# Kernel optimization log

Measured on AMD Instinct MI355X. Metric: run time of the kernel, lower is better.

## Reference

```python
import jax, jax.numpy as jnp
import numpy as np

H = 128          # hidden_size
D2 = 2 * H       # mod / q_enc channels
D8 = 8 * H       # att channels
B, S, G, Q = 16, 4096, 24, 48
WIN = 12         # +/- window half-width from source


def _masked_softmax(s, m, axis):
    s = jnp.where(m.astype(bool), s, jnp.float32(-1e30))
    return jax.nn.softmax(s, axis=axis)


def _bidaf(c, q, c_mask, q_mask, c_w, q_w, cq_w, bias):
    # c: [B,Lc,D2], q: [B,Lq,D2]; eval mode -> dropout is identity
    s0 = c @ c_w                                  # [B,Lc,1]
    s1 = (q @ q_w).transpose(0, 2, 1)             # [B,1,Lq]
    s2 = jnp.einsum('bcd,bqd->bcq', c * cq_w, q)  # [B,Lc,Lq]
    s = s0 + s1 + s2 + bias
    sm1 = _masked_softmax(s, q_mask[:, None, :], 2)
    sm2 = _masked_softmax(s, c_mask[:, :, None], 1)
    a = jnp.einsum('bcq,bqd->bcd', sm1, q)
    ss = jnp.einsum('bcq,bkq->bck', sm1, sm2)     # s1 @ s2^T
    b = jnp.einsum('bck,bkd->bcd', ss, c)
    return jnp.concatenate([c, a, c * a, c * b], axis=-1)  # [B,Lc,4*D2]


def setup_inputs() -> dict:
    key = jax.random.key(0)
    ks = jax.random.split(key, 12)
    inp = {
        'att': jax.random.normal(ks[0], (B, S, D8), jnp.float32),
        'mod': jax.random.normal(ks[1], (B, S, D2), jnp.float32),
        'q_enc': jax.random.normal(ks[2], (B, Q, D2), jnp.float32),
        'gap_indices': jnp.sort(jax.random.randint(ks[3], (B, G), 0, S), axis=1).astype(jnp.int32),
        'mask': jnp.ones((B, S), jnp.int32),
        'q_mask': jnp.ones((B, Q), jnp.int32),
        'c_w': jax.random.normal(ks[4], (D2, 1), jnp.float32) * 0.05,
        'q_w': jax.random.normal(ks[5], (D2, 1), jnp.float32) * 0.05,
        'cq_w': jax.random.normal(ks[6], (D2,), jnp.float32) * 0.05,
        'att_bias': jnp.zeros((1,), jnp.float32),
        'W_att': jax.random.normal(ks[7], (3 * D8, 1), jnp.float32) * 0.02,
        'b_att': jnp.zeros((1,), jnp.float32),
        'W_mod': jax.random.normal(ks[8], (3 * D2, 1), jnp.float32) * 0.02,
        'b_mod': jnp.zeros((1,), jnp.float32),
        'W_att2': jax.random.normal(ks[9], (D8, 1), jnp.float32) * 0.02,
        'b_att2': jnp.zeros((1,), jnp.float32),
        'W_att_s': jax.random.normal(ks[10], (3 * D8, 1), jnp.float32) * 0.02,
        'b_att_s': jnp.zeros((1,), jnp.float32),
        'W_mod_s': jax.random.normal(ks[11], (3 * D2, 1), jnp.float32) * 0.02,
        'b_mod_s': jnp.zeros((1,), jnp.float32),
        'W_att_s2': jax.random.normal(jax.random.fold_in(key, 99), (D8, 1), jnp.float32) * 0.02,
        'b_att_s2': jnp.zeros((1,), jnp.float32),
    }
    return inp


def reference(att, mod, q_enc, gap_indices, mask, q_mask,
              c_w, q_w, cq_w, att_bias,
              W_att, b_att, W_mod, b_mod, W_att2, b_att2,
              W_att_s, b_att_s, W_mod_s, b_mod_s, W_att_s2, b_att_s2):
    batch, seq_len, _ = mod.shape
    idxb = jnp.arange(batch)[:, None]
    att_gaps = att[idxb, gap_indices]   # [B,G,D8]
    mod_gaps = mod[idxb, gap_indices]   # [B,G,D2]

    att_2 = _bidaf(mod_gaps, q_enc, jnp.ones_like(gap_indices), q_mask,
                   c_w, q_w, cq_w, att_bias)  # [B,G,8h]

    # gap 0: full-sequence pooling (max is unmasked in the source; avg uses mask sum)
    denom0 = jnp.sum(mask.astype(jnp.float32), axis=1)[:, None]
    p0_mod = jnp.concatenate([jnp.max(mod, axis=1), jnp.sum(mod, axis=1) / denom0], axis=-1)[:, None]
    p0_att = jnp.concatenate([jnp.max(att, axis=1), jnp.sum(att, axis=1) / denom0], axis=-1)[:, None]

    pos = jnp.arange(seq_len)[None, :]
    mask_b = mask.astype(bool)

    def step(carry, gid):  # gid: [B]
        wm = (pos >= gid[:, None] - WIN) & (pos <= gid[:, None] + WIN) & mask_b
        wmf = wm.astype(jnp.float32)                 # [B,S]
        den = jnp.sum(wmf, axis=1)[:, None]          # [B,1]
        mw = mod * wmf[:, :, None]
        aw = att * wmf[:, :, None]
        pm = jnp.concatenate([jnp.max(mw, axis=1), jnp.sum(mw, axis=1) / den], axis=-1)
        pa = jnp.concatenate([jnp.max(aw, axis=1), jnp.sum(aw, axis=1) / den], axis=-1)
        return carry, (pm, pa)

    _, (pm, pa) = jax.lax.scan(step, None, gap_indices[:, 1:].T)  # [G-1,B,*]
    pools_mod = jnp.concatenate([p0_mod, pm.transpose(1, 0, 2)], axis=1)  # [B,G,4h]
    pools_att = jnp.concatenate([p0_att, pa.transpose(1, 0, 2)], axis=1)  # [B,G,16h]

    mod_g = jnp.concatenate([mod_gaps, pools_mod], axis=-1)  # [B,G,6h]
    att_g = jnp.concatenate([att_gaps, pools_att], axis=-1)  # [B,G,24h]

    lin = lambda x, W, b: x @ W + b
    logit0 = lin(att_g[:, :1], W_att_s, b_att_s) + lin(mod_g[:, :1], W_mod_s, b_mod_s) + lin(att_2[:, :1], W_att_s2, b_att_s2)
    logits = lin(att_g[:, 1:], W_att, b_att) + lin(mod_g[:, 1:], W_mod, b_mod) + lin(att_2[:, 1:], W_att2, b_att2)
    return jnp.concatenate([logit0, logits], axis=1).squeeze(-1)  # [B,G]
```

## Files before the change

### kernel.cpp

```cpp
#include <hip/hip_runtime.h>
#include <math.h>

#define BATCH 16
#define S_LEN 4096
#define D2c   256
#define D8c   1024
#define GNUM  24
#define QNUM  48
#define WINc  12
#define NCA   64
#define NCM   16
#define NSB   (BATCH * GNUM)
#define NWB   (BATCH * (GNUM - 1))

__device__ inline float4 f4max(float4 a, float4 b) {
    return make_float4(fmaxf(a.x,b.x), fmaxf(a.y,b.y), fmaxf(a.z,b.z), fmaxf(a.w,b.w));
}
__device__ inline float4 f4add(float4 a, float4 b) {
    return make_float4(a.x+b.x, a.y+b.y, a.z+b.z, a.w+b.w);
}
__device__ inline float4 f4scale(float4 a, float s) {
    return make_float4(a.x*s, a.y*s, a.z*s, a.w*s);
}
__device__ inline float4 f4mul(float4 a, float4 b) {
    return make_float4(a.x*b.x, a.y*b.y, a.z*b.z, a.w*b.w);
}
__device__ inline float dot4(float4 a, float4 b) {
    return a.x*b.x + a.y*b.y + a.z*b.z + a.w*b.w;
}
__device__ inline unsigned fmap(float x) {
    unsigned u = __float_as_uint(x);
    return (u >> 31) ? ~u : (u | 0x80000000u);
}
__device__ inline float funmap(unsigned u) {
    return (u >> 31) ? __uint_as_float(u & 0x7FFFFFFFu) : __uint_as_float(~u);
}

struct SSh {
    float c[D2c];
    float pa[4][QNUM];
    float pb[4][QNUM];
    float pm[8][32];
    float p0[2][64];
    int   gids[GNUM];
};
struct WSh {
    float wmf[32];
    float red[256];
    float rden;
};
union ShU { SSh s; WSh w; };

__global__ __launch_bounds__(256) void k1_kernel(
    const float* __restrict__ att, const float* __restrict__ mod,
    const float* __restrict__ q_enc,
    const int* __restrict__ gap_idx, const int* __restrict__ mask,
    const float* __restrict__ c_w, const float* __restrict__ cq_w,
    const float* __restrict__ W_att2, const float* __restrict__ W_att_s2,
    const float* __restrict__ W_att, const float* __restrict__ W_mod,
    const float* __restrict__ W_att_s, const float* __restrict__ W_mod_s,
    unsigned* __restrict__ attMaxU, unsigned* __restrict__ modMaxU,
    float* __restrict__ sumdots,
    float* __restrict__ s2v_ws, float* __restrict__ vv_ws,
    float* __restrict__ m_ws, float* __restrict__ s0uc_ws,
    float* __restrict__ winpart)
{
    __shared__ ShU sh;
    const int tid = threadIdx.x;
    const int bid = blockIdx.x;

    if (bid < NSB) {
        const int b = bid / GNUM, g = bid % GNUM;
        const float4* mod4 = reinterpret_cast<const float4*>(mod);
        const float4* q4   = reinterpret_cast<const float4*>(q_enc);
        const float4* Wsel = reinterpret_cast<const float4*>((g == 0) ? W_att_s2 : W_att2);

        if (tid < GNUM) sh.s.gids[tid] = gap_idx[b * GNUM + tid];
        __syncthreads();
        const int gid = sh.s.gids[g];
        if (tid < 64)
            reinterpret_cast<float4*>(sh.s.c)[tid] = mod4[((size_t)b * S_LEN + gid) * (D2c/4) + tid];
        __syncthreads();
        const float4* c4 = reinterpret_cast<const float4*>(sh.s.c);

        if (tid < 64) {
            sh.s.p0[0][tid] = dot4(c4[tid], reinterpret_cast<const float4*>(c_w)[tid]);
        } else if (tid < 128) {
            sh.s.p0[1][tid - 64] = dot4(c4[tid - 64], Wsel[tid - 64]);
        }

        {
            const int q = tid & 63, p = tid >> 6;
            if (q < QNUM) {
                const float4* qr = q4 + ((size_t)b * QNUM + q) * (D2c/4) + p * 16;
                const float4* cl = c4 + p * 16;
                const float4* cw = reinterpret_cast<const float4*>(cq_w) + p * 16;
                const float4* wa = Wsel + 2 * (D2c/4) + p * 16;
                float a_s2 = 0.f, a_v = 0.f;
                #pragma unroll
                for (int i = 0; i < 16; ++i) {
                    const float4 cq = f4mul(cl[i], qr[i]);
                    a_s2 += dot4(cq, cw[i]);
                    a_v  += dot4(cq, wa[i]);
                }
                sh.s.pa[p][q] = a_s2;
                sh.s.pb[p][q] = a_v;
            }
        }

        {
            const int k = tid & 31, p8 = tid >> 5;
            if (k < GNUM) {
                const float4* kr = mod4 + ((size_t)b * S_LEN + sh.s.gids[k]) * (D2c/4) + p8 * 8;
                const float4* cl = c4 + p8 * 8;
                const float4* wb = Wsel + 3 * (D2c/4) + p8 * 8;
                float am = 0.f;
                #pragma unroll
                for (int i = 0; i < 8; ++i) {
                    const float4 t = f4mul(cl[i], kr[i]);
                    am += dot4(t, wb[i]);
                }
                sh.s.pm[p8][k] = am;
            }
        }
        __syncthreads();

        if (tid < QNUM) {
            const float s2 = sh.s.pa[0][tid] + sh.s.pa[1][tid] + sh.s.pa[2][tid] + sh.s.pa[3][tid];
            const float v  = sh.s.pb[0][tid] + sh.s.pb[1][tid] + sh.s.pb[2][tid] + sh.s.pb[3][tid];
            s2v_ws[(size_t)bid * QNUM + tid] = s2;
            vv_ws [(size_t)bid * QNUM + tid] = v;
        } else if (tid >= 64 && tid < 64 + GNUM) {
            const int k = tid - 64;
            float m = 0.f;
            #pragma unroll
            for (int p8 = 0; p8 < 8; ++p8) m += sh.s.pm[p8][k];
            m_ws[(size_t)bid * GNUM + k] = m;
        } else if (tid == 62) {
            float a = 0.f;
            for (int i = 0; i < 64; ++i) a += sh.s.p0[0][i];
            s0uc_ws[(size_t)bid * 2 + 0] = a;
        } else if (tid == 63) {
            float a = 0.f;
            for (int i = 0; i < 64; ++i) a += sh.s.p0[1][i];
            s0uc_ws[(size_t)bid * 2 + 1] = a;
        }
    } else if (bid < NSB + NWB) {
        const int wb = bid - NSB;
        const int b = wb / (GNUM - 1), g = wb % (GNUM - 1) + 1;
        const int gid = gap_idx[b * GNUM + g];
        const int lo = (gid - WINc > 0) ? gid - WINc : 0;
        const int hi = (gid + WINc < S_LEN - 1) ? gid + WINc : S_LEN - 1;
        const int n = hi - lo + 1;
        const int gsel = gid - lo;

        if (tid < 32)
            sh.w.wmf[tid] = (tid < n && mask[b * S_LEN + lo + tid] != 0) ? 1.f : 0.f;
        __syncthreads();
        if (tid == 0) {
            float d = 0.f;
            for (int i = 0; i < 25; ++i) d += sh.w.wmf[i];
            sh.w.rden = 1.f / d;
        }
        __syncthreads();
        const float rden = sh.w.rden;

        const float4* Wa4 = reinterpret_cast<const float4*>(W_att);
        const float4* Wm4 = reinterpret_cast<const float4*>(W_mod);

        float acc = 0.f;
        {
            const float4* base = reinterpret_cast<const float4*>(att)
                                 + ((size_t)b * S_LEN + lo) * (D8c/4) + tid;
            float4 mx = make_float4(0.f, 0.f, 0.f, 0.f);
            float4 sm = make_float4(0.f, 0.f, 0.f, 0.f);
            float4 gv = make_float4(0.f, 0.f, 0.f, 0.f);
            #pragma unroll 5
            for (int i = 0; i < 25; ++i) {
                const int off = (i < n) ? i : 0;
                const float4 v = base[(size_t)off * (D8c/4)];
                const float w = sh.w.wmf[i];
                const float4 vm = f4scale(v, w);
                mx = f4max(mx, vm);
                sm = f4add(sm, vm);
                if (i == gsel) gv = v;
            }
            acc += dot4(gv, Wa4[tid]);
            acc += dot4(mx, Wa4[(D8c/4) + tid]) + dot4(sm, Wa4[2*(D8c/4) + tid]) * rden;
        }
        if (tid < D2c/4) {
            const float4* base = reinterpret_cast<const float4*>(mod)
                                 + ((size_t)b * S_LEN + lo) * (D2c/4) + tid;
            float4 mx = make_float4(0.f, 0.f, 0.f, 0.f);
            float4 sm = make_float4(0.f, 0.f, 0.f, 0.f);
            float4 gv = make_float4(0.f, 0.f, 0.f, 0.f);
            #pragma unroll 5
            for (int i = 0; i < 25; ++i) {
                const int off = (i < n) ? i : 0;
                const float4 v = base[(size_t)off * (D2c/4)];
                const float w = sh.w.wmf[i];
                const float4 vm = f4scale(v, w);
                mx = f4max(mx, vm);
                sm = f4add(sm, vm);
                if (i == gsel) gv = v;
            }
            acc += dot4(gv, Wm4[tid]);
            acc += dot4(mx, Wm4[(D2c/4) + tid]) + dot4(sm, Wm4[2*(D2c/4) + tid]) * rden;
        }

        sh.w.red[tid] = acc;
        __syncthreads();
        for (int off = 128; off > 0; off >>= 1) {
            if (tid < off) sh.w.red[tid] += sh.w.red[tid + off];
            __syncthreads();
        }
        if (tid == 0) winpart[b * GNUM + g] = sh.w.red[0];
    } else if (bid < NSB + NWB + BATCH * NCA) {
        const int ab = bid - NSB - NWB;
        const int b = ab >> 6, ch = ab & 63;
        const float4* base = reinterpret_cast<const float4*>(att)
                             + ((size_t)b * S_LEN + ch * 64) * (D8c/4) + tid;
        float4 mx = make_float4(-INFINITY, -INFINITY, -INFINITY, -INFINITY);
        float4 sm = make_float4(0.f, 0.f, 0.f, 0.f);
        #pragma unroll 8
        for (int r = 0; r < 64; ++r) {
            const float4 v = base[(size_t)r * (D8c/4)];
            mx = f4max(mx, v);
            sm = f4add(sm, v);
        }
        unsigned* amax = attMaxU + (size_t)b * D8c + tid * 4;
        atomicMax(&amax[0], fmap(mx.x));
        atomicMax(&amax[1], fmap(mx.y));
        atomicMax(&amax[2], fmap(mx.z));
        atomicMax(&amax[3], fmap(mx.w));
        const float4 wsum = reinterpret_cast<const float4*>(W_att_s)[2*(D8c/4) + tid];
        sh.w.red[tid] = dot4(sm, wsum);
        __syncthreads();
        for (int off = 128; off > 0; off >>= 1) {
            if (tid < off) sh.w.red[tid] += sh.w.red[tid + off];
            __syncthreads();
        }
        if (tid == 0) atomicAdd(&sumdots[b], sh.w.red[0]);
    } else {
        const int mb = bid - NSB - NWB - BATCH * NCA;
        const int b = mb >> 4, ch = mb & 15;
        const int rg = tid >> 6, c4i = tid & 63;
        const float4* base = reinterpret_cast<const float4*>(mod)
                             + ((size_t)b * S_LEN + ch * 256 + rg * 64) * (D2c/4) + c4i;
        float4 mx = make_float4(-INFINITY, -INFINITY, -INFINITY, -INFINITY);
        float4 sm = make_float4(0.f, 0.f, 0.f, 0.f);
        #pragma unroll 8
        for (int r = 0; r < 64; ++r) {
            const float4 v = base[(size_t)r * (D2c/4)];
            mx = f4max(mx, v);
            sm = f4add(sm, v);
        }
        unsigned* mmax = modMaxU + (size_t)b * D2c + c4i * 4;
        atomicMax(&mmax[0], fmap(mx.x));
        atomicMax(&mmax[1], fmap(mx.y));
        atomicMax(&mmax[2], fmap(mx.z));
        atomicMax(&mmax[3], fmap(mx.w));
        const float4 wsum = reinterpret_cast<const float4*>(W_mod_s)[2*(D2c/4) + c4i];
        sh.w.red[tid] = dot4(sm, wsum);
        __syncthreads();
        for (int off = 128; off > 0; off >>= 1) {
            if (tid < off) sh.w.red[tid] += sh.w.red[tid + off];
            __syncthreads();
        }
        if (tid == 0) atomicAdd(&sumdots[BATCH + b], sh.w.red[0]);
    }
}

__global__ __launch_bounds__(256) void k2_kernel(
    const float* __restrict__ att, const float* __restrict__ mod,
    const float* __restrict__ q_enc,
    const int* __restrict__ gap_idx, const int* __restrict__ mask,
    const int* __restrict__ q_mask,
    const float* __restrict__ q_w, const float* __restrict__ att_bias,
    const float* __restrict__ W_att2, const float* __restrict__ W_att_s2,
    const float* __restrict__ W_att_s, const float* __restrict__ W_mod_s,
    const float* __restrict__ b_att, const float* __restrict__ b_mod,
    const float* __restrict__ b_att2,
    const float* __restrict__ b_att_s, const float* __restrict__ b_mod_s,
    const float* __restrict__ b_att_s2,
    const unsigned* __restrict__ attMaxU, const unsigned* __restrict__ modMaxU,
    const float* __restrict__ sumdots,
    const float* __restrict__ s2v_ws, const float* __restrict__ vv_ws,
    const float* __restrict__ m_ws, const float* __restrict__ s0uc_ws,
    const float* __restrict__ winpart,
    float* __restrict__ out)
{
    const int b = blockIdx.x;
    const int tid = threadIdx.x;

    __shared__ float s_sh[GNUM][QNUM];
    __shared__ float sm1[GNUM][QNUM];
    __shared__ float sm2[GNUM][QNUM];
    __shared__ float ssm[GNUM][GNUM];
    __shared__ float pq[3][4][QNUM];
    __shared__ float s1[QNUM], u0[QNUM], u1[QNUM];
    __shared__ float s0g[GNUM], ucg[GNUM], att2v[GNUM];
    __shared__ float red[256];
    __shared__ float rdensh;

    {
        const int q = tid & 63, p = tid >> 6;
        if (q < QNUM) {
            const float4* qr = reinterpret_cast<const float4*>(q_enc)
                               + ((size_t)b * QNUM + q) * (D2c/4) + p * 16;
            const float4* w1 = reinterpret_cast<const float4*>(q_w) + p * 16;
            const float4* w2 = reinterpret_cast<const float4*>(W_att_s2) + (D2c/4) + p * 16;
            const float4* w3 = reinterpret_cast<const float4*>(W_att2)   + (D2c/4) + p * 16;
            float a1 = 0.f, a2 = 0.f, a3 = 0.f;
            #pragma unroll
            for (int i = 0; i < 16; ++i) {
                const float4 v = qr[i];
                a1 += dot4(v, w1[i]);
                a2 += dot4(v, w2[i]);
                a3 += dot4(v, w3[i]);
            }
            pq[0][p][q] = a1; pq[1][p][q] = a2; pq[2][p][q] = a3;
        }
    }
    if (tid < GNUM) {
        s0g[tid] = s0uc_ws[((size_t)b * GNUM + tid) * 2 + 0];
        ucg[tid] = s0uc_ws[((size_t)b * GNUM + tid) * 2 + 1];
    }
    __syncthreads();
    if (tid < QNUM) {
        s1[tid] = pq[0][0][tid] + pq[0][1][tid] + pq[0][2][tid] + pq[0][3][tid];
        u0[tid] = pq[1][0][tid] + pq[1][1][tid] + pq[1][2][tid] + pq[1][3][tid];
        u1[tid] = pq[2][0][tid] + pq[2][1][tid] + pq[2][2][tid] + pq[2][3][tid];
    }
    __syncthreads();

    const float bias = att_bias[0];
    for (int i = tid; i < GNUM * QNUM; i += 256) {
        const int g = i / QNUM, q = i % QNUM;
        s_sh[g][q] = s0g[g] + s1[q] + s2v_ws[((size_t)b * GNUM + g) * QNUM + q] + bias;
    }
    __syncthreads();

    if (tid < QNUM) {
        const int q = tid;
        float mxv = -1e30f;
        for (int g = 0; g < GNUM; ++g) mxv = fmaxf(mxv, s_sh[g][q]);
        float sum = 0.f;
        for (int g = 0; g < GNUM; ++g) {
            const float e = __expf(s_sh[g][q] - mxv);
            sm2[g][q] = e;
            sum += e;
        }
        const float inv = 1.f / sum;
        for (int g = 0; g < GNUM; ++g) sm2[g][q] *= inv;
    } else if (tid >= 64 && tid < 64 + GNUM) {
        const int g = tid - 64;
        float mxv = -1e30f;
        for (int q = 0; q < QNUM; ++q)
            if (q_mask[b * QNUM + q]) mxv = fmaxf(mxv, s_sh[g][q]);
        float sum = 0.f;
        for (int q = 0; q < QNUM; ++q) {
            const float e = q_mask[b * QNUM + q] ? __expf(s_sh[g][q] - mxv) : 0.f;
            sm1[g][q] = e;
            sum += e;
        }
        const float inv = 1.f / sum;
        for (int q = 0; q < QNUM; ++q) sm1[g][q] *= inv;
    }
    __syncthreads();

    for (int i = tid; i < GNUM * GNUM; i += 256) {
        const int g = i / GNUM, k = i % GNUM;
        float t = 0.f;
        for (int q = 0; q < QNUM; ++q) t += sm1[g][q] * sm2[k][q];
        ssm[g][k] = t * m_ws[((size_t)b * GNUM + g) * GNUM + k];
    }
    __syncthreads();

    if (tid < GNUM) {
        const int g = tid;
        const float* uu = (g == 0) ? u0 : u1;
        float acc = ucg[g];
        for (int q = 0; q < QNUM; ++q)
            acc += sm1[g][q] * (uu[q] + vv_ws[((size_t)b * GNUM + g) * QNUM + q]);
        for (int k = 0; k < GNUM; ++k) acc += ssm[g][k];
        att2v[g] = acc;
    }

    float cnt = 0.f;
    for (int s = tid; s < S_LEN; s += 256) cnt += (mask[b * S_LEN + s] != 0) ? 1.f : 0.f;
    red[tid] = cnt;
    __syncthreads();
    for (int off = 128; off > 0; off >>= 1) {
        if (tid < off) red[tid] += red[tid + off];
        __syncthreads();
    }
    if (tid == 0) rdensh = 1.f / red[0];
    __syncthreads();
    const float rden0 = rdensh;

    const int gid0 = gap_idx[b * GNUM];
    const float4* Wa4 = reinterpret_cast<const float4*>(W_att_s);
    const float4* Wm4 = reinterpret_cast<const float4*>(W_mod_s);

    float acc = 0.f;
    {
        const uint4 mu = reinterpret_cast<const uint4*>(attMaxU + (size_t)b * D8c)[tid];
        const float4 mx = make_float4(funmap(mu.x), funmap(mu.y), funmap(mu.z), funmap(mu.w));
        acc += dot4(mx, Wa4[(D8c/4) + tid]);
        const float4 ar = reinterpret_cast<const float4*>(att)[((size_t)b * S_LEN + gid0) * (D8c/4) + tid];
        acc += dot4(ar, Wa4[tid]);
    }
    if (tid < D2c/4) {
        const uint4 mu = reinterpret_cast<const uint4*>(modMaxU + (size_t)b * D2c)[tid];
        const float4 mx = make_float4(funmap(mu.x), funmap(mu.y), funmap(mu.z), funmap(mu.w));
        acc += dot4(mx, Wm4[(D2c/4) + tid]);
        const float4 mr = reinterpret_cast<const float4*>(mod)[((size_t)b * S_LEN + gid0) * (D2c/4) + tid];
        acc += dot4(mr, Wm4[tid]);
    }

    __syncthreads();
    red[tid] = acc;
    __syncthreads();
    for (int off = 128; off > 0; off >>= 1) {
        if (tid < off) red[tid] += red[tid + off];
        __syncthreads();
    }
    if (tid == 0) {
        const float avgpart = (sumdots[b] + sumdots[BATCH + b]) * rden0;
        out[b * GNUM] = red[0] + avgpart + att2v[0] + b_att_s[0] + b_mod_s[0] + b_att_s2[0];
    } else if (tid < GNUM) {
        out[b * GNUM + tid] = winpart[b * GNUM + tid] + att2v[tid]
                              + b_att[0] + b_mod[0] + b_att2[0];
    }
}

extern "C" void kernel_launch(void* const* d_in, const int* in_sizes, int n_in,
                              void* d_out, int out_size, void* d_ws, size_t ws_size,
                              hipStream_t stream)
{
    const float* att      = (const float*)d_in[0];
    const float* mod      = (const float*)d_in[1];
    const float* q_enc    = (const float*)d_in[2];
    const int*   gap_idx  = (const int*)  d_in[3];
    const int*   mask     = (const int*)  d_in[4];
    const int*   q_mask   = (const int*)  d_in[5];
    const float* c_w      = (const float*)d_in[6];
    const float* q_w      = (const float*)d_in[7];
    const float* cq_w     = (const float*)d_in[8];
    const float* att_bias = (const float*)d_in[9];
    const float* W_att    = (const float*)d_in[10];
    const float* b_att    = (const float*)d_in[11];
    const float* W_mod    = (const float*)d_in[12];
    const float* b_mod    = (const float*)d_in[13];
    const float* W_att2   = (const float*)d_in[14];
    const float* b_att2   = (const float*)d_in[15];
    const float* W_att_s  = (const float*)d_in[16];
    const float* b_att_s  = (const float*)d_in[17];
    const float* W_mod_s  = (const float*)d_in[18];
    const float* b_mod_s  = (const float*)d_in[19];
    const float* W_att_s2 = (const float*)d_in[20];
    const float* b_att_s2 = (const float*)d_in[21];

    float* out = (float*)d_out;

    unsigned* attMaxU = (unsigned*)d_ws;
    unsigned* modMaxU = attMaxU + (size_t)BATCH * D8c;
    float*    sumdots = (float*)(modMaxU + (size_t)BATCH * D2c);
    float*    s2v_ws  = sumdots + 32;
    float*    vv_ws   = s2v_ws + (size_t)NSB * QNUM;
    float*    m_ws    = vv_ws  + (size_t)NSB * QNUM;
    float*    s0uc_ws = m_ws   + (size_t)NSB * GNUM;
    float*    winpart = s0uc_ws + (size_t)NSB * 2;

    const size_t atomicBytes = ((size_t)BATCH * D8c + (size_t)BATCH * D2c + 32) * 4;
    hipMemsetAsync(d_ws, 0, atomicBytes, stream);

    const int grid1 = NSB + NWB + BATCH*NCA + BATCH*NCM;

    k1_kernel<<<grid1, 256, 0, stream>>>(
        att, mod, q_enc, gap_idx, mask,
        c_w, cq_w, W_att2, W_att_s2, W_att, W_mod, W_att_s, W_mod_s,
        attMaxU, modMaxU, sumdots,
        s2v_ws, vv_ws, m_ws, s0uc_ws, winpart);

    k2_kernel<<<BATCH, 256, 0, stream>>>(
        att, mod, q_enc, gap_idx, mask, q_mask,
        q_w, att_bias, W_att2, W_att_s2,
        W_att_s, W_mod_s, b_att, b_mod, b_att2,
        b_att_s, b_mod_s, b_att_s2,
        attMaxU, modMaxU, sumdots,
        s2v_ws, vv_ws, m_ws, s0uc_ws, winpart, out);
}
```

Baseline: 100.9 us.

## Reorder block roles, double streaming chunks, use nontemporal loads and wave shuffles

Moves the bandwidth-heavy att/mod streaming blocks to the front of the grid, ahead of the small gap and window blocks. It halves the rows per block so twice as many chunks run. Loads now use nontemporal hints, and the shared-memory tree reductions are replaced with wave-level shuffle reductions plus one atomic per wave. The aim is better HBM streaming and less synchronisation, at the cost of more atomicMax and atomicAdd traffic.

```diff
diff --git a/kernel.cpp b/kernel.cpp
--- a/kernel.cpp
+++ b/kernel.cpp
@@ -8,10 +8,14 @@
 #define GNUM  24
 #define QNUM  48
 #define WINc  12
-#define NCA   64
-#define NCM   16
+#define NCA   128
+#define NCM   32
 #define NSB   (BATCH * GNUM)
 #define NWB   (BATCH * (GNUM - 1))
+#define N_ATT (BATCH * NCA)
+#define N_MOD (BATCH * NCM)
+
+typedef float floatx4 __attribute__((ext_vector_type(4)));
 
 __device__ inline float4 f4max(float4 a, float4 b) {
     return make_float4(fmaxf(a.x,b.x), fmaxf(a.y,b.y), fmaxf(a.z,b.z), fmaxf(a.w,b.w));
@@ -27,6 +31,10 @@
 }
 __device__ inline float dot4(float4 a, float4 b) {
     return a.x*b.x + a.y*b.y + a.z*b.z + a.w*b.w;
+}
+__device__ inline float4 ldnt4(const float4* p) {
+    const floatx4 v = __builtin_nontemporal_load(reinterpret_cast<const floatx4*>(p));
+    return make_float4(v.x, v.y, v.z, v.w);
 }
 __device__ inline unsigned fmap(float x) {
     unsigned u = __float_as_uint(x);
@@ -34,6 +42,11 @@
 }
 __device__ inline float funmap(unsigned u) {
     return (u >> 31) ? __uint_as_float(u & 0x7FFFFFFFu) : __uint_as_float(~u);
+}
+__device__ inline float wredsum(float v) {
+    #pragma unroll
+    for (int m = 32; m > 0; m >>= 1) v += __shfl_xor(v, m, 64);
+    return v;
 }
 
 struct SSh {
@@ -69,84 +82,50 @@
     const int tid = threadIdx.x;
     const int bid = blockIdx.x;
 
-    if (bid < NSB) {
-        const int b = bid / GNUM, g = bid % GNUM;
-        const float4* mod4 = reinterpret_cast<const float4*>(mod);
-        const float4* q4   = reinterpret_cast<const float4*>(q_enc);
-        const float4* Wsel = reinterpret_cast<const float4*>((g == 0) ? W_att_s2 : W_att2);
-
-        if (tid < GNUM) sh.s.gids[tid] = gap_idx[b * GNUM + tid];
-        __syncthreads();
-        const int gid = sh.s.gids[g];
-        if (tid < 64)
-            reinterpret_cast<float4*>(sh.s.c)[tid] = mod4[((size_t)b * S_LEN + gid) * (D2c/4) + tid];
-        __syncthreads();
-        const float4* c4 = reinterpret_cast<const float4*>(sh.s.c);
-
-        if (tid < 64) {
-            sh.s.p0[0][tid] = dot4(c4[tid], reinterpret_cast<const float4*>(c_w)[tid]);
-        } else if (tid < 128) {
-            sh.s.p0[1][tid - 64] = dot4(c4[tid - 64], Wsel[tid - 64]);
-        }
-
-        {
-            const int q = tid & 63, p = tid >> 6;
-            if (q < QNUM) {
-                const float4* qr = q4 + ((size_t)b * QNUM + q) * (D2c/4) + p * 16;
-                const float4* cl = c4 + p * 16;
-                const float4* cw = reinterpret_cast<const float4*>(cq_w) + p * 16;
-                const float4* wa = Wsel + 2 * (D2c/4) + p * 16;
-                float a_s2 = 0.f, a_v = 0.f;
-                #pragma unroll
-                for (int i = 0; i < 16; ++i) {
-                    const float4 cq = f4mul(cl[i], qr[i]);
-                    a_s2 += dot4(cq, cw[i]);
-                    a_v  += dot4(cq, wa[i]);
-                }
-                sh.s.pa[p][q] = a_s2;
-                sh.s.pb[p][q] = a_v;
-            }
-        }
-
-        {
-            const int k = tid & 31, p8 = tid >> 5;
-            if (k < GNUM) {
-                const float4* kr = mod4 + ((size_t)b * S_LEN + sh.s.gids[k]) * (D2c/4) + p8 * 8;
-                const float4* cl = c4 + p8 * 8;
-                const float4* wb = Wsel + 3 * (D2c/4) + p8 * 8;
-                float am = 0.f;
-                #pragma unroll
-                for (int i = 0; i < 8; ++i) {
-                    const float4 t = f4mul(cl[i], kr[i]);
-                    am += dot4(t, wb[i]);
-                }
-                sh.s.pm[p8][k] = am;
-            }
-        }
-        __syncthreads();
-
-        if (tid < QNUM) {
-            const float s2 = sh.s.pa[0][tid] + sh.s.pa[1][tid] + sh.s.pa[2][tid] + sh.s.pa[3][tid];
-            const float v  = sh.s.pb[0][tid] + sh.s.pb[1][tid] + sh.s.pb[2][tid] + sh.s.pb[3][tid];
-            s2v_ws[(size_t)bid * QNUM + tid] = s2;
-            vv_ws [(size_t)bid * QNUM + tid] = v;
-        } else if (tid >= 64 && tid < 64 + GNUM) {
-            const int k = tid - 64;
-            float m = 0.f;
-            #pragma unroll
-            for (int p8 = 0; p8 < 8; ++p8) m += sh.s.pm[p8][k];
-            m_ws[(size_t)bid * GNUM + k] = m;
-        } else if (tid == 62) {
-            float a = 0.f;
-            for (int i = 0; i < 64; ++i) a += sh.s.p0[0][i];
-            s0uc_ws[(size_t)bid * 2 + 0] = a;
-        } else if (tid == 63) {
-            float a = 0.f;
-            for (int i = 0; i < 64; ++i) a += sh.s.p0[1][i];
-            s0uc_ws[(size_t)bid * 2 + 1] = a;
-        }
-    } else if (bid < NSB + NWB) {
-        const int wb = bid - NSB;
+    if (bid < N_ATT) {
+        const int b = bid >> 7, ch = bid & 127;
+        const float4* base = reinterpret_cast<const float4*>(att)
+                             + ((size_t)b * S_LEN + ch * 32) * (D8c/4) + tid;
+        float4 mx = make_float4(-INFINITY, -INFINITY, -INFINITY, -INFINITY);
+        float4 sm = make_float4(0.f, 0.f, 0.f, 0.f);
+        #pragma unroll 16
+        for (int r = 0; r < 32; ++r) {
+            const float4 v = ldnt4(base + (size_t)r * (D8c/4));
+            mx = f4max(mx, v);
+            sm = f4add(sm, v);
+        }
+        unsigned* amax = attMaxU + (size_t)b * D8c + tid * 4;
+        atomicMax(&amax[0], fmap(mx.x));
+        atomicMax(&amax[1], fmap(mx.y));
+        atomicMax(&amax[2], fmap(mx.z));
+        atomicMax(&amax[3], fmap(mx.w));
+        const float4 wsum = reinterpret_cast<const float4*>(W_att_s)[2*(D8c/4) + tid];
+        const float p = wredsum(dot4(sm, wsum));
+        if ((tid & 63) == 0) atomicAdd(&sumdots[b], p);
+    } else if (bid < N_ATT + N_MOD) {
+        const int mb = bid - N_ATT;
+        const int b = mb >> 5, ch = mb & 31;
+        const int rg = tid >> 6, c4i = tid & 63;
+        const float4* base = reinterpret_cast<const float4*>(mod)
+                             + ((size_t)b * S_LEN + ch * 128 + rg * 32) * (D2c/4) + c4i;
+        float4 mx = make_float4(-INFINITY, -INFINITY, -INFINITY, -INFINITY);
+        float4 sm = make_float4(0.f, 0.f, 0.f, 0.f);
+        #pragma unroll 16
+        for (int r = 0; r < 32; ++r) {
+            const float4 v = ldnt4(base + (size_t)r * (D2c/4));
+            mx = f4max(mx, v);
+            sm = f4add(sm, v);
+        }
+        unsigned* mmax = modMaxU + (size_t)b * D2c + c4i * 4;
+        atomicMax(&mmax[0], fmap(mx.x));
+        atomicMax(&mmax[1], fmap(mx.y));
+        atomicMax(&mmax[2], fmap(mx.z));
+        atomicMax(&mmax[3], fmap(mx.w));
+        const float4 wsum = reinterpret_cast<const float4*>(W_mod_s)[2*(D2c/4) + c4i];
+        const float p = wredsum(dot4(sm, wsum));
+        if ((tid & 63) == 0) atomicAdd(&sumdots[BATCH + b], p);
+    } else if (bid < N_ATT + N_MOD + NWB) {
+        const int wb = bid - N_ATT - N_MOD;
         const int b = wb / (GNUM - 1), g = wb % (GNUM - 1) + 1;
         const int gid = gap_idx[b * GNUM + g];
         const int lo = (gid - WINc > 0) ? gid - WINc : 0;
@@ -215,59 +194,83 @@
             __syncthreads();
         }
         if (tid == 0) winpart[b * GNUM + g] = sh.w.red[0];
-    } else if (bid < NSB + NWB + BATCH * NCA) {
-        const int ab = bid - NSB - NWB;
-        const int b = ab >> 6, ch = ab & 63;
-        const float4* base = reinterpret_cast<const float4*>(att)
-                             + ((size_t)b * S_LEN + ch * 64) * (D8c/4) + tid;
-        float4 mx = make_float4(-INFINITY, -INFINITY, -INFINITY, -INFINITY);
-        float4 sm = make_float4(0.f, 0.f, 0.f, 0.f);
-        #pragma unroll 8
-        for (int r = 0; r < 64; ++r) {
-            const float4 v = base[(size_t)r * (D8c/4)];
-            mx = f4max(mx, v);
-            sm = f4add(sm, v);
-        }
-        unsigned* amax = attMaxU + (size_t)b * D8c + tid * 4;
-        atomicMax(&amax[0], fmap(mx.x));
-        atomicMax(&amax[1], fmap(mx.y));
-        atomicMax(&amax[2], fmap(mx.z));
-        atomicMax(&amax[3], fmap(mx.w));
-        const float4 wsum = reinterpret_cast<const float4*>(W_att_s)[2*(D8c/4) + tid];
-        sh.w.red[tid] = dot4(sm, wsum);
-        __syncthreads();
-        for (int off = 128; off > 0; off >>= 1) {
-            if (tid < off) sh.w.red[tid] += sh.w.red[tid + off];
-            __syncthreads();
-        }
-        if (tid == 0) atomicAdd(&sumdots[b], sh.w.red[0]);
     } else {
-        const int mb = bid - NSB - NWB - BATCH * NCA;
-        const int b = mb >> 4, ch = mb & 15;
-        const int rg = tid >> 6, c4i = tid & 63;
-        const float4* base = reinterpret_cast<const float4*>(mod)
-                             + ((size_t)b * S_LEN + ch * 256 + rg * 64) * (D2c/4) + c4i;
-        float4 mx = make_float4(-INFINITY, -INFINITY, -INFINITY, -INFINITY);
-        float4 sm = make_float4(0.f, 0.f, 0.f, 0.f);
-        #pragma unroll 8
-        for (int r = 0; r < 64; ++r) {
-            const float4 v = base[(size_t)r * (D2c/4)];
-            mx = f4max(mx, v);
-            sm = f4add(sm, v);
-        }
-        unsigned* mmax = modMaxU + (size_t)b * D2c + c4i * 4;
-        atomicMax(&mmax[0], fmap(mx.x));
-        atomicMax(&mmax[1], fmap(mx.y));
-        atomicMax(&mmax[2], fmap(mx.z));
-        atomicMax(&mmax[3], fmap(mx.w));
-        const float4 wsum = reinterpret_cast<const float4*>(W_mod_s)[2*(D2c/4) + c4i];
-        sh.w.red[tid] = dot4(sm, wsum);
-        __syncthreads();
-        for (int off = 128; off > 0; off >>= 1) {
-            if (tid < off) sh.w.red[tid] += sh.w.red[tid + off];
-            __syncthreads();
-        }
-        if (tid == 0) atomicAdd(&sumdots[BATCH + b], sh.w.red[0]);
+        const int sb = bid - N_ATT - N_MOD - NWB;
+        const int b = sb / GNUM, g = sb % GNUM;
+        const float4* mod4 = reinterpret_cast<const float4*>(mod);
+        const float4* q4   = reinterpret_cast<const float4*>(q_enc);
+        const float4* Wsel = reinterpret_cast<const float4*>((g == 0) ? W_att_s2 : W_att2);
+
+        if (tid < GNUM) sh.s.gids[tid] = gap_idx[b * GNUM + tid];
+        __syncthreads();
+        const int gid = sh.s.gids[g];
+        if (tid < 64)
+            reinterpret_cast<float4*>(sh.s.c)[tid] = mod4[((size_t)b * S_LEN + gid) * (D2c/4) + tid];
+        __syncthreads();
+        const float4* c4 = reinterpret_cast<const float4*>(sh.s.c);
+
+        if (tid < 64) {
+            sh.s.p0[0][tid] = dot4(c4[tid], reinterpret_cast<const float4*>(c_w)[tid]);
+        } else if (tid < 128) {
+            sh.s.p0[1][tid - 64] = dot4(c4[tid - 64], Wsel[tid - 64]);
+        }
+
+        {
+            const int q = tid & 63, p = tid >> 6;
+            if (q < QNUM) {
+                const float4* qr = q4 + ((size_t)b * QNUM + q) * (D2c/4) + p * 16;
+                const float4* cl = c4 + p * 16;
+                const float4* cw = reinterpret_cast<const float4*>(cq_w) + p * 16;
+                const float4* wa = Wsel + 2 * (D2c/4) + p * 16;
+                float a_s2 = 0.f, a_v = 0.f;
+                #pragma unroll
+                for (int i = 0; i < 16; ++i) {
+                    const float4 cq = f4mul(cl[i], qr[i]);
+                    a_s2 += dot4(cq, cw[i]);
+                    a_v  += dot4(cq, wa[i]);
+                }
+                sh.s.pa[p][q] = a_s2;
+                sh.s.pb[p][q] = a_v;
+            }
+        }
+
+        {
+            const int k = tid & 31, p8 = tid >> 5;
+            if (k < GNUM) {
+                const float4* kr = mod4 + ((size_t)b * S_LEN + sh.s.gids[k]) * (D2c/4) + p8 * 8;
+                const float4* cl = c4 + p8 * 8;
+                const float4* wb = Wsel + 3 * (D2c/4) + p8 * 8;
+                float am = 0.f;
+                #pragma unroll
+                for (int i = 0; i < 8; ++i) {
+                    const float4 t = f4mul(cl[i], kr[i]);
+                    am += dot4(t, wb[i]);
+                }
+                sh.s.pm[p8][k] = am;
+            }
+        }
+        __syncthreads();
+
+        if (tid < QNUM) {
+            const float s2 = sh.s.pa[0][tid] + sh.s.pa[1][tid] + sh.s.pa[2][tid] + sh.s.pa[3][tid];
+            const float v  = sh.s.pb[0][tid] + sh.s.pb[1][tid] + sh.s.pb[2][tid] + sh.s.pb[3][tid];
+            s2v_ws[(size_t)sb * QNUM + tid] = s2;
+            vv_ws [(size_t)sb * QNUM + tid] = v;
+        } else if (tid >= 64 && tid < 64 + GNUM) {
+            const int k = tid - 64;
+            float m = 0.f;
+            #pragma unroll
+            for (int p8 = 0; p8 < 8; ++p8) m += sh.s.pm[p8][k];
+            m_ws[(size_t)sb * GNUM + k] = m;
+        } else if (tid == 62) {
+            float a = 0.f;
+            for (int i = 0; i < 64; ++i) a += sh.s.p0[0][i];
+            s0uc_ws[(size_t)sb * 2 + 0] = a;
+        } else if (tid == 63) {
+            float a = 0.f;
+            for (int i = 0; i < 64; ++i) a += sh.s.p0[1][i];
+            s0uc_ws[(size_t)sb * 2 + 1] = a;
+        }
     }
 }
 
@@ -474,9 +477,9 @@
     float*    winpart = s0uc_ws + (size_t)NSB * 2;
 
     const size_t atomicBytes = ((size_t)BATCH * D8c + (size_t)BATCH * D2c + 32) * 4;
-    hipMemsetAsync(d_ws, 0, atomicBytes, stream);
-
-    const int grid1 = NSB + NWB + BATCH*NCA + BATCH*NCM;
+    (void)hipMemsetAsync(d_ws, 0, atomicBytes, stream);
+
+    const int grid1 = N_ATT + N_MOD + NWB + NSB;
 
     k1_kernel<<<grid1, 256, 0, stream>>>(
         att, mod, q_enc, gap_idx, mask,
```

After: 178.3 us. +76.7%, slower.
